# Kernel optimization log

Measured on AMD Instinct MI355X. Metric: run time of the kernel, lower is better.

Reference implementation:

```python
import jax, jax.numpy as jnp
import numpy as np

NU = 50000   # n_users
NI = 50000   # n_items
N = NU + NI  # total nodes in the square normalized adjacency
D = 64       # emb_dim
K = 4        # number of sub-graphs in hypergraph_list
E = 1000000  # interactions per sub-graph (symmetrized -> 2E nnz)


def setup_inputs() -> dict:
    key = jax.random.key(0)
    ks = jax.random.split(key, 9)
    stdv = 1.0 / np.sqrt(D)
    return {
        "x": jax.random.normal(ks[0], (N, D), jnp.float32),
        "hgc1_bias": jax.random.uniform(ks[1], (D,), jnp.float32, -stdv, stdv),
        "fc1_W": jax.random.normal(ks[2], (D, D), jnp.float32) * stdv,
        "fus_l1_W": jax.random.normal(ks[3], (D, D), jnp.float32) * stdv,
        "fus_l1_b": jnp.zeros((D,), jnp.float32),
        "fus_l2_W": jax.random.normal(ks[4], (1, D), jnp.float32) * stdv,
        "fus_l2_b": jnp.zeros((1,), jnp.float32),
        "rows": jax.random.randint(ks[5], (K, E), 0, NU),
        "cols": jax.random.randint(ks[6], (K, E), 0, NI),
    }


def reference(x, hgc1_bias, fc1_W, fus_l1_W, fus_l1_b, fus_l2_W, fus_l2_b, rows, cols):
    def spmm(src, dst, val, h):
        # (L @ h)[i] = sum over nnz (src=i): val * h[dst]
        return jax.ops.segment_sum(val[:, None] * h[dst], src, num_segments=N)

    def step(xc, rc):
        r, c = rc
        # symmetric bipartite adjacency A (items offset by NU)
        src = jnp.concatenate([r, c + NU])  # (2E,)
        dst = jnp.concatenate([c + NU, r])  # (2E,)
        # D^-1/2 A D^-1/2  (degree = row nnz count, as in (A>0).sum)
        deg = jax.ops.segment_sum(jnp.ones(src.shape, jnp.float32), src, num_segments=N) + 1e-7
        dinv = deg ** -0.5
        val = dinv[src] * dinv[dst]
        # HGNN2: relu -> hgc1 (bias add, edge=G^T x, x=G edge; G symmetric) -> softmax -> fc1
        h = jax.nn.relu(xc) + hgc1_bias
        edge = spmm(src, dst, val, h)
        node = spmm(src, dst, val, edge)
        node = jax.nn.softmax(node, axis=1)
        node = node @ fc1_W.T  # fc1 has no bias
        # Fusion gate (dropout off in eval)
        emb = jnp.stack([xc, node])  # (2, N, D)
        score = jax.nn.softmax(
            jnp.tanh(emb @ fus_l1_W.T + fus_l1_b) @ fus_l2_W.T + fus_l2_b, axis=0
        )  # (2, N, 1)
        x_new = jnp.sum(score * emb, axis=0)
        return x_new, (x_new, edge)

    _, (nodes, edges) = jax.lax.scan(step, x, (rows, cols))
    # embedding_list[sub_key] = [x, edge] per sub-graph -> stacked (K, N, D)
    return nodes, edges
```

## Files before the change

### kernel.cpp

```cpp
#include <hip/hip_runtime.h>
#include <hip/hip_bf16.h>

#define NU_ 50000
#define NI_ 50000
#define NN  (NU_ + NI_)
#define DD  64
#define KK  4
#define EE  1000000
#define SCAN_B ((NN + 255) / 256)

#define P_RANGES 8
#define RANGE_SZ ((NN + P_RANGES - 1) / P_RANGES)

__global__ __launch_bounds__(256) void k_hist(const int* __restrict__ rows,
                                              const int* __restrict__ cols,
                                              int* __restrict__ cnt4) {
    const int k = blockIdx.y;
    int e = blockIdx.x * 256 + threadIdx.x;
    if (e >= EE) return;
    int a = rows[(size_t)k * EE + e], b = cols[(size_t)k * EE + e];
    if ((unsigned)a >= (unsigned)NU_ || (unsigned)b >= (unsigned)NI_) return;
    int* cnt = cnt4 + (size_t)k * NN;
    atomicAdd(&cnt[a], 1);
    atomicAdd(&cnt[NU_ + b], 1);
}

__global__ __launch_bounds__(256) void k_bsum(const int* __restrict__ cnt4,
                                              int* __restrict__ bsum4) {
    __shared__ int s[256];
    const int k = blockIdx.y;
    int i = blockIdx.x * 256 + threadIdx.x;
    s[threadIdx.x] = (i < NN) ? cnt4[(size_t)k * NN + i] : 0;
    __syncthreads();
    #pragma unroll
    for (int off = 128; off > 0; off >>= 1) {
        if (threadIdx.x < off) s[threadIdx.x] += s[threadIdx.x + off];
        __syncthreads();
    }
    if (threadIdx.x == 0) bsum4[k * SCAN_B + blockIdx.x] = s[0];
}

__global__ __launch_bounds__(512) void k_sscan(const int* __restrict__ bsum4,
                                               int* __restrict__ bofs4) {
    __shared__ int s[512];
    const int k = blockIdx.x;
    int tid = threadIdx.x;
    s[tid] = (tid < SCAN_B) ? bsum4[k * SCAN_B + tid] : 0;
    __syncthreads();
    #pragma unroll
    for (int off = 1; off < 512; off <<= 1) {
        int v = (tid >= off) ? s[tid - off] : 0;
        __syncthreads();
        s[tid] += v;
        __syncthreads();
    }
    if (tid < SCAN_B) bofs4[k * SCAN_B + tid] = (tid > 0) ? s[tid - 1] : 0;
}

__global__ __launch_bounds__(256) void k_apply(const int* __restrict__ cnt4,
                                               const int* __restrict__ bofs4,
                                               int* __restrict__ row_ptr4,
                                               int* __restrict__ cursor4,
                                               float* __restrict__ dinv4) {
    __shared__ int s[256];
    const int k = blockIdx.y;
    int i = blockIdx.x * 256 + threadIdx.x;
    int v = (i < NN) ? cnt4[(size_t)k * NN + i] : 0;
    s[threadIdx.x] = v;
    __syncthreads();
    #pragma unroll
    for (int off = 1; off < 256; off <<= 1) {
        int t = (threadIdx.x >= off) ? s[threadIdx.x - off] : 0;
        __syncthreads();
        s[threadIdx.x] += t;
        __syncthreads();
    }
    if (i < NN) {
        int incl = s[threadIdx.x] + bofs4[k * SCAN_B + blockIdx.x];
        int excl = incl - v;
        row_ptr4[(size_t)k * (NN + 1) + i] = excl;
        cursor4[(size_t)k * NN + i] = excl;
        dinv4[(size_t)k * NN + i] = rsqrtf((float)v + 1e-7f);
        if (i == NN - 1) row_ptr4[(size_t)k * (NN + 1) + NN] = incl;
    }
}

__global__ __launch_bounds__(256) void k_scatter2(const int* __restrict__ rows,
                                                  const int* __restrict__ cols,
                                                  int* __restrict__ cursor4,
                                                  int* __restrict__ adj4) {
    const int g = blockIdx.x;
    const int k = blockIdx.z;
    const int lo = g * RANGE_SZ;
    int e = blockIdx.y * 256 + threadIdx.x;
    if (e >= EE) return;
    int a = rows[(size_t)k * EE + e], b = cols[(size_t)k * EE + e];
    if ((unsigned)a >= (unsigned)NU_ || (unsigned)b >= (unsigned)NI_) return;
    b += NU_;
    int* cursor = cursor4 + (size_t)k * NN;
    int* adj = adj4 + (size_t)k * 2 * EE;
    if ((unsigned)(a - lo) < (unsigned)RANGE_SZ) {
        int p = atomicAdd(&cursor[a], 1);
        adj[p] = b;
    }
    if ((unsigned)(b - lo) < (unsigned)RANGE_SZ) {
        int q = atomicAdd(&cursor[b], 1);
        adj[q] = a;
    }
}

__global__ __launch_bounds__(256) void k_prep(const float* __restrict__ x,
                                              const float* __restrict__ bias,
                                              const float* __restrict__ dinv,
                                              float* __restrict__ hbuf) {
    int i = blockIdx.x * 256 + threadIdx.x;
    int node = i >> 4;
    float dv = dinv[node];
    const float4 xv = ((const float4*)x)[i];
    const float4 bv = ((const float4*)bias)[i & 15];
    float4 o;
    o.x = dv * (fmaxf(xv.x, 0.f) + bv.x);
    o.y = dv * (fmaxf(xv.y, 0.f) + bv.y);
    o.z = dv * (fmaxf(xv.z, 0.f) + bv.z);
    o.w = dv * (fmaxf(xv.w, 0.f) + bv.w);
    ((float4*)hbuf)[i] = o;
}

__global__ __launch_bounds__(256) void k_pullA(const int* __restrict__ row_ptr,
                                               const int* __restrict__ adj,
                                               const float* __restrict__ dinv,
                                               const float* __restrict__ hbuf,
                                               float* __restrict__ out_e,
                                               float* __restrict__ h2buf) {
    const int wave = threadIdx.x >> 6;
    const int lane = threadIdx.x & 63;
    const int sub  = lane >> 4;
    const int l16  = lane & 15;
    const int lb   = sub << 4;
    const int row  = (blockIdx.x * 4 + wave) * 4 + sub;
    const int start = row_ptr[row];
    const int end   = row_ptr[row + 1];
    float4 aA = {0,0,0,0}, aB = {0,0,0,0};
    for (int base = start; base < end; base += 16) {
        int n = end - base; if (n > 16) n = 16;
        int idx = (l16 < n) ? adj[base + l16] : 0;
        int j = 0;
        for (; j + 3 < n; j += 4) {
            int n0 = __shfl(idx, lb | j);
            int n1 = __shfl(idx, lb | (j + 1));
            int n2 = __shfl(idx, lb | (j + 2));
            int n3 = __shfl(idx, lb | (j + 3));
            const float4 v0 = *(const float4*)&hbuf[(size_t)n0 * DD + l16 * 4];
            const float4 v1 = *(const float4*)&hbuf[(size_t)n1 * DD + l16 * 4];
            const float4 v2 = *(const float4*)&hbuf[(size_t)n2 * DD + l16 * 4];
            const float4 v3 = *(const float4*)&hbuf[(size_t)n3 * DD + l16 * 4];
            aA.x += v0.x; aA.y += v0.y; aA.z += v0.z; aA.w += v0.w;
            aB.x += v1.x; aB.y += v1.y; aB.z += v1.z; aB.w += v1.w;
            aA.x += v2.x; aA.y += v2.y; aA.z += v2.z; aA.w += v2.w;
            aB.x += v3.x; aB.y += v3.y; aB.z += v3.z; aB.w += v3.w;
        }
        for (; j < n; j++) {
            int nb = __shfl(idx, lb | j);
            const float4 v = *(const float4*)&hbuf[(size_t)nb * DD + l16 * 4];
            aA.x += v.x; aA.y += v.y; aA.z += v.z; aA.w += v.w;
        }
    }
    float4 acc = {aA.x + aB.x, aA.y + aB.y, aA.z + aB.z, aA.w + aB.w};
    const float dr = dinv[row];
    float4 e = {dr * acc.x, dr * acc.y, dr * acc.z, dr * acc.w};
    *(float4*)&out_e[(size_t)row * DD + l16 * 4] = e;
    float4 e2 = {dr * e.x, dr * e.y, dr * e.z, dr * e.w};
    *(float4*)&h2buf[(size_t)row * DD + l16 * 4] = e2;
}

__global__ __launch_bounds__(256) void k_pullB(const int* __restrict__ row_ptr,
                                               const int* __restrict__ adj,
                                               const float* __restrict__ dinv,
                                               const float* __restrict__ h2buf,
                                               float* __restrict__ out_n) {
    const int wave = threadIdx.x >> 6;
    const int lane = threadIdx.x & 63;
    const int sub  = lane >> 4;
    const int l16  = lane & 15;
    const int lb   = sub << 4;
    const int row  = (blockIdx.x * 4 + wave) * 4 + sub;
    const int start = row_ptr[row];
    const int end   = row_ptr[row + 1];
    float4 aA = {0,0,0,0}, aB = {0,0,0,0};
    for (int base = start; base < end; base += 16) {
        int n = end - base; if (n > 16) n = 16;
        int idx = (l16 < n) ? adj[base + l16] : 0;
        int j = 0;
        for (; j + 3 < n; j += 4) {
            int n0 = __shfl(idx, lb | j);
            int n1 = __shfl(idx, lb | (j + 1));
            int n2 = __shfl(idx, lb | (j + 2));
            int n3 = __shfl(idx, lb | (j + 3));
            const float4 v0 = *(const float4*)&h2buf[(size_t)n0 * DD + l16 * 4];
            const float4 v1 = *(const float4*)&h2buf[(size_t)n1 * DD + l16 * 4];
            const float4 v2 = *(const float4*)&h2buf[(size_t)n2 * DD + l16 * 4];
            const float4 v3 = *(const float4*)&h2buf[(size_t)n3 * DD + l16 * 4];
            aA.x += v0.x; aA.y += v0.y; aA.z += v0.z; aA.w += v0.w;
            aB.x += v1.x; aB.y += v1.y; aB.z += v1.z; aB.w += v1.w;
            aA.x += v2.x; aA.y += v2.y; aA.z += v2.z; aA.w += v2.w;
            aB.x += v3.x; aB.y += v3.y; aB.z += v3.z; aB.w += v3.w;
        }
        for (; j < n; j++) {
            int nb = __shfl(idx, lb | j);
            const float4 v = *(const float4*)&h2buf[(size_t)nb * DD + l16 * 4];
            aA.x += v.x; aA.y += v.y; aA.z += v.z; aA.w += v.w;
        }
    }
    float4 acc = {aA.x + aB.x, aA.y + aB.y, aA.z + aB.z, aA.w + aB.w};
    const float dr = dinv[row];
    float4 o = {dr * acc.x, dr * acc.y, dr * acc.z, dr * acc.w};
    *(float4*)&out_n[(size_t)row * DD + l16 * 4] = o;
}

#define BC(v, d) __uint_as_float(__builtin_amdgcn_readlane(__float_as_uint(v), (d)))

__global__ __launch_bounds__(256) void k_row(
    const float* __restrict__ node, const float* __restrict__ xsrc,
    const float* __restrict__ fc1W, const float* __restrict__ fusW,
    const float* __restrict__ l1b, const float* __restrict__ l2w,
    const float* __restrict__ l2b, const float* __restrict__ hgb,
    const float* __restrict__ dinv_next, float* __restrict__ out_nodes,
    float* __restrict__ hbuf_next) {
    const int wave = threadIdx.x >> 6;
    const int lane = threadIdx.x & 63;

    float wf[DD], wu[DD];
    #pragma unroll
    for (int d = 0; d < DD; d += 4) {
        *(float4*)&wf[d] = *(const float4*)&fc1W[(size_t)lane * DD + d];
        *(float4*)&wu[d] = *(const float4*)&fusW[(size_t)lane * DD + d];
    }
    const float b1v = l1b[lane];
    const float l2v = l2w[lane];
    const float b2v = l2b[0];
    const float hgv = hgb[lane];

    for (int row = blockIdx.x * 4 + wave; row < NN; row += gridDim.x * 4) {
        const size_t base = (size_t)row * DD + lane;
        float v = node[base];
        float m = v;
        #pragma unroll
        for (int s = 1; s < 64; s <<= 1) m = fmaxf(m, __shfl_xor(m, s));
        float ev = __expf(v - m);
        float sum = ev;
        #pragma unroll
        for (int s = 1; s < 64; s <<= 1) sum += __shfl_xor(sum, s);
        float sm = ev / sum;
        float n0 = 0, n1 = 0, n2 = 0, n3 = 0;
        #pragma unroll
        for (int d = 0; d < DD; d += 4) {
            n0 = fmaf(BC(sm, d),     wf[d],     n0);
            n1 = fmaf(BC(sm, d + 1), wf[d + 1], n1);
            n2 = fmaf(BC(sm, d + 2), wf[d + 2], n2);
            n3 = fmaf(BC(sm, d + 3), wf[d + 3], n3);
        }
        float nf = (n0 + n1) + (n2 + n3);
        float xc = xsrc[base];
        float a0 = 0, a1 = 0, a2 = 0, a3 = 0;
        #pragma unroll
        for (int d = 0; d < DD; d += 4) {
            a0 = fmaf(BC(xc, d),     wu[d],     a0);
            a1 = fmaf(BC(xc, d + 1), wu[d + 1], a1);
            a2 = fmaf(BC(xc, d + 2), wu[d + 2], a2);
            a3 = fmaf(BC(xc, d + 3), wu[d + 3], a3);
        }
        float tt = tanhf(((a0 + a1) + (a2 + a3)) + b1v);
        float p = tt * l2v;
        #pragma unroll
        for (int s = 1; s < 64; s <<= 1) p += __shfl_xor(p, s);
        float s_x = p + b2v;
        a0 = 0; a1 = 0; a2 = 0; a3 = 0;
        #pragma unroll
        for (int d = 0; d < DD; d += 4) {
            a0 = fmaf(BC(nf, d),     wu[d],     a0);
            a1 = fmaf(BC(nf, d + 1), wu[d + 1], a1);
            a2 = fmaf(BC(nf, d + 2), wu[d + 2], a2);
            a3 = fmaf(BC(nf, d + 3), wu[d + 3], a3);
        }
        tt = tanhf(((a0 + a1) + (a2 + a3)) + b1v);
        p = tt * l2v;
        #pragma unroll
        for (int s = 1; s < 64; s <<= 1) p += __shfl_xor(p, s);
        float s_n = p + b2v;
        float mm = fmaxf(s_x, s_n);
        float e0 = __expf(s_x - mm), e1 = __expf(s_n - mm);
        float inv = 1.0f / (e0 + e1);
        float xn = (e0 * xc + e1 * nf) * inv;
        out_nodes[base] = xn;
        if (hbuf_next) {
            float dv = dinv_next[row];
            hbuf_next[base] = dv * (fmaxf(xn, 0.f) + hgv);
        }
    }
}

extern "C" void kernel_launch(void* const* d_in, const int* in_sizes, int n_in,
                              void* d_out, int out_size, void* d_ws, size_t ws_size,
                              hipStream_t stream) {
    const float* x    = (const float*)d_in[0];
    const float* b1   = (const float*)d_in[1];
    const float* fc1W = (const float*)d_in[2];
    const float* fusW = (const float*)d_in[3];
    const float* l1b  = (const float*)d_in[4];
    const float* l2w  = (const float*)d_in[5];
    const float* l2b  = (const float*)d_in[6];
    const int* rows = (const int*)d_in[7];
    const int* cols = (const int*)d_in[8];
    float* out = (float*)d_out;

    const int ND = NN * DD;

    float* hbuf     = (float*)d_ws;
    float* h2buf    = hbuf + (size_t)NN * DD;
    float* dinv4    = h2buf + (size_t)NN * DD;
    int*   cnt4     = (int*)(dinv4 + (size_t)4 * NN);
    int*   row_ptr4 = cnt4 + (size_t)4 * NN;
    int*   cursor4  = row_ptr4 + (size_t)4 * (NN + 1);
    int*   bsum4    = cursor4 + (size_t)4 * NN;
    int*   bofs4    = bsum4 + 4 * SCAN_B;
    int*   adj4     = bofs4 + 4 * SCAN_B;

    hipMemsetAsync(cnt4, 0, (size_t)4 * NN * sizeof(int), stream);
    {
        dim3 g((EE + 255) / 256, KK);
        k_hist<<<g, 256, 0, stream>>>(rows, cols, cnt4);
    }
    {
        dim3 g(SCAN_B, KK);
        k_bsum<<<g, 256, 0, stream>>>(cnt4, bsum4);
    }
    k_sscan<<<KK, 512, 0, stream>>>(bsum4, bofs4);
    {
        dim3 g(SCAN_B, KK);
        k_apply<<<g, 256, 0, stream>>>(cnt4, bofs4, row_ptr4, cursor4, dinv4);
    }
    {
        dim3 g(P_RANGES, (EE + 255) / 256, KK);
        k_scatter2<<<g, 256, 0, stream>>>(rows, cols, cursor4, adj4);
    }

    k_prep<<<ND / 4 / 256, 256, 0, stream>>>(x, b1, dinv4, hbuf);

    for (int k = 0; k < KK; k++) {
        const int*   rp = row_ptr4 + (size_t)k * (NN + 1);
        const int*   aj = adj4 + (size_t)k * 2 * EE;
        const float* dv = dinv4 + (size_t)k * NN;
        const float* xk = (k == 0) ? x : out + (size_t)(k - 1) * ND;
        float* out_n = out + (size_t)k * ND;
        float* out_e = out + (size_t)(KK + k) * ND;

        k_pullA<<<NN / 16, 256, 0, stream>>>(rp, aj, dv, hbuf, out_e, h2buf);

        k_pullB<<<NN / 16, 256, 0, stream>>>(rp, aj, dv, h2buf, out_n);

        const float* dvn = (k < KK - 1) ? dinv4 + (size_t)(k + 1) * NN : nullptr;
        float* hbn = (k < KK - 1) ? hbuf : nullptr;
        k_row<<<1024, 256, 0, stream>>>(out_n, xk, fc1W, fusW, l1b, l2w, l2b,
                                        b1, dvn, out_n, hbn);
    }
}
```

Baseline: 1.793 ms.

## Range-partition histogram atomics, split scatter launches, widen gather accumulators

The degree histogram is now partitioned over node ranges like the scatter, so each block only issues atomics for nodes in its range, which improves atomic locality in cache. The scatter is split into two launches of two sub-graphs each. The SpMM gather loop gets a fully unrolled path for full 16-neighbour chunks and four independent accumulators to raise memory-level parallelism. In exchange, the histogram rereads the edge list once per range, and the extra accumulators raise register pressure.

```diff
diff --git a/kernel.cpp b/kernel.cpp
--- a/kernel.cpp
+++ b/kernel.cpp
@@ -12,17 +12,20 @@
 #define P_RANGES 8
 #define RANGE_SZ ((NN + P_RANGES - 1) / P_RANGES)
 
-__global__ __launch_bounds__(256) void k_hist(const int* __restrict__ rows,
-                                              const int* __restrict__ cols,
-                                              int* __restrict__ cnt4) {
-    const int k = blockIdx.y;
-    int e = blockIdx.x * 256 + threadIdx.x;
+__global__ __launch_bounds__(256) void k_hist2(const int* __restrict__ rows,
+                                               const int* __restrict__ cols,
+                                               int* __restrict__ cnt4) {
+    const int g = blockIdx.x;
+    const int k = blockIdx.z;
+    const int lo = g * RANGE_SZ;
+    int e = blockIdx.y * 256 + threadIdx.x;
     if (e >= EE) return;
     int a = rows[(size_t)k * EE + e], b = cols[(size_t)k * EE + e];
     if ((unsigned)a >= (unsigned)NU_ || (unsigned)b >= (unsigned)NI_) return;
+    b += NU_;
     int* cnt = cnt4 + (size_t)k * NN;
-    atomicAdd(&cnt[a], 1);
-    atomicAdd(&cnt[NU_ + b], 1);
+    if ((unsigned)(a - lo) < (unsigned)RANGE_SZ) atomicAdd(&cnt[a], 1);
+    if ((unsigned)(b - lo) < (unsigned)RANGE_SZ) atomicAdd(&cnt[b], 1);
 }
 
 __global__ __launch_bounds__(256) void k_bsum(const int* __restrict__ cnt4,
@@ -88,9 +91,10 @@
 __global__ __launch_bounds__(256) void k_scatter2(const int* __restrict__ rows,
                                                   const int* __restrict__ cols,
                                                   int* __restrict__ cursor4,
-                                                  int* __restrict__ adj4) {
+                                                  int* __restrict__ adj4,
+                                                  int kbase) {
     const int g = blockIdx.x;
-    const int k = blockIdx.z;
+    const int k = kbase + blockIdx.z;
     const int lo = g * RANGE_SZ;
     int e = blockIdx.y * 256 + threadIdx.x;
     if (e >= EE) return;
@@ -126,6 +130,55 @@
     ((float4*)hbuf)[i] = o;
 }
 
+#define GATHER_ROW(SRC, accOut)                                                \
+    float4 aA = {0,0,0,0}, aB = {0,0,0,0}, aC = {0,0,0,0}, aD = {0,0,0,0};     \
+    for (int base = start; base < end; base += 16) {                           \
+        int n = end - base; if (n > 16) n = 16;                                \
+        int idx = (l16 < n) ? adj[base + l16] : 0;                             \
+        if (n == 16) {                                                         \
+            _Pragma("unroll")                                                  \
+            for (int j = 0; j < 16; j += 4) {                                  \
+                int n0 = __shfl(idx, lb | j);                                  \
+                int n1 = __shfl(idx, lb | (j + 1));                            \
+                int n2 = __shfl(idx, lb | (j + 2));                            \
+                int n3 = __shfl(idx, lb | (j + 3));                            \
+                const float4 v0 = *(const float4*)&SRC[(size_t)n0 * DD + l16 * 4]; \
+                const float4 v1 = *(const float4*)&SRC[(size_t)n1 * DD + l16 * 4]; \
+                const float4 v2 = *(const float4*)&SRC[(size_t)n2 * DD + l16 * 4]; \
+                const float4 v3 = *(const float4*)&SRC[(size_t)n3 * DD + l16 * 4]; \
+                aA.x += v0.x; aA.y += v0.y; aA.z += v0.z; aA.w += v0.w;        \
+                aB.x += v1.x; aB.y += v1.y; aB.z += v1.z; aB.w += v1.w;        \
+                aC.x += v2.x; aC.y += v2.y; aC.z += v2.z; aC.w += v2.w;        \
+                aD.x += v3.x; aD.y += v3.y; aD.z += v3.z; aD.w += v3.w;        \
+            }                                                                  \
+        } else {                                                               \
+            int j = 0;                                                         \
+            for (; j + 3 < n; j += 4) {                                        \
+                int n0 = __shfl(idx, lb | j);                                  \
+                int n1 = __shfl(idx, lb | (j + 1));                            \
+                int n2 = __shfl(idx, lb | (j + 2));                            \
+                int n3 = __shfl(idx, lb | (j + 3));                            \
+                const float4 v0 = *(const float4*)&SRC[(size_t)n0 * DD + l16 * 4]; \
+                const float4 v1 = *(const float4*)&SRC[(size_t)n1 * DD + l16 * 4]; \
+                const float4 v2 = *(const float4*)&SRC[(size_t)n2 * DD + l16 * 4]; \
+                const float4 v3 = *(const float4*)&SRC[(size_t)n3 * DD + l16 * 4]; \
+                aA.x += v0.x; aA.y += v0.y; aA.z += v0.z; aA.w += v0.w;        \
+                aB.x += v1.x; aB.y += v1.y; aB.z += v1.z; aB.w += v1.w;        \
+                aC.x += v2.x; aC.y += v2.y; aC.z += v2.z; aC.w += v2.w;        \
+                aD.x += v3.x; aD.y += v3.y; aD.z += v3.z; aD.w += v3.w;        \
+            }                                                                  \
+            for (; j < n; j++) {                                               \
+                int nb = __shfl(idx, lb | j);                                  \
+                const float4 v = *(const float4*)&SRC[(size_t)nb * DD + l16 * 4]; \
+                aA.x += v.x; aA.y += v.y; aA.z += v.z; aA.w += v.w;            \
+            }                                                                  \
+        }                                                                      \
+    }                                                                          \
+    float4 accOut = {(aA.x + aB.x) + (aC.x + aD.x),                            \
+                     (aA.y + aB.y) + (aC.y + aD.y),                            \
+                     (aA.z + aB.z) + (aC.z + aD.z),                            \
+                     (aA.w + aB.w) + (aC.w + aD.w)};
+
 __global__ __launch_bounds__(256) void k_pullA(const int* __restrict__ row_ptr,
                                                const int* __restrict__ adj,
                                                const float* __restrict__ dinv,
@@ -140,32 +193,7 @@
     const int row  = (blockIdx.x * 4 + wave) * 4 + sub;
     const int start = row_ptr[row];
     const int end   = row_ptr[row + 1];
-    float4 aA = {0,0,0,0}, aB = {0,0,0,0};
-    for (int base = start; base < end; base += 16) {
-        int n = end - base; if (n > 16) n = 16;
-        int idx = (l16 < n) ? adj[base + l16] : 0;
-        int j = 0;
-        for (; j + 3 < n; j += 4) {
-            int n0 = __shfl(idx, lb | j);
-            int n1 = __shfl(idx, lb | (j + 1));
-            int n2 = __shfl(idx, lb | (j + 2));
-            int n3 = __shfl(idx, lb | (j + 3));
-            const float4 v0 = *(const float4*)&hbuf[(size_t)n0 * DD + l16 * 4];
-            const float4 v1 = *(const float4*)&hbuf[(size_t)n1 * DD + l16 * 4];
-            const float4 v2 = *(const float4*)&hbuf[(size_t)n2 * DD + l16 * 4];
-            const float4 v3 = *(const float4*)&hbuf[(size_t)n3 * DD + l16 * 4];
-            aA.x += v0.x; aA.y += v0.y; aA.z += v0.z; aA.w += v0.w;
-            aB.x += v1.x; aB.y += v1.y; aB.z += v1.z; aB.w += v1.w;
-            aA.x += v2.x; aA.y += v2.y; aA.z += v2.z; aA.w += v2.w;
-            aB.x += v3.x; aB.y += v3.y; aB.z += v3.z; aB.w += v3.w;
-        }
-        for (; j < n; j++) {
-            int nb = __shfl(idx, lb | j);
-            const float4 v = *(const float4*)&hbuf[(size_t)nb * DD + l16 * 4];
-            aA.x += v.x; aA.y += v.y; aA.z += v.z; aA.w += v.w;
-        }
-    }
-    float4 acc = {aA.x + aB.x, aA.y + aB.y, aA.z + aB.z, aA.w + aB.w};
+    GATHER_ROW(hbuf, acc)
     const float dr = dinv[row];
     float4 e = {dr * acc.x, dr * acc.y, dr * acc.z, dr * acc.w};
     *(float4*)&out_e[(size_t)row * DD + l16 * 4] = e;
@@ -186,32 +214,7 @@
     const int row  = (blockIdx.x * 4 + wave) * 4 + sub;
     const int start = row_ptr[row];
     const int end   = row_ptr[row + 1];
-    float4 aA = {0,0,0,0}, aB = {0,0,0,0};
-    for (int base = start; base < end; base += 16) {
-        int n = end - base; if (n > 16) n = 16;
-        int idx = (l16 < n) ? adj[base + l16] : 0;
-        int j = 0;
-        for (; j + 3 < n; j += 4) {
-            int n0 = __shfl(idx, lb | j);
-            int n1 = __shfl(idx, lb | (j + 1));
-            int n2 = __shfl(idx, lb | (j + 2));
-            int n3 = __shfl(idx, lb | (j + 3));
-            const float4 v0 = *(const float4*)&h2buf[(size_t)n0 * DD + l16 * 4];
-            const float4 v1 = *(const float4*)&h2buf[(size_t)n1 * DD + l16 * 4];
-            const float4 v2 = *(const float4*)&h2buf[(size_t)n2 * DD + l16 * 4];
-            const float4 v3 = *(const float4*)&h2buf[(size_t)n3 * DD + l16 * 4];
-            aA.x += v0.x; aA.y += v0.y; aA.z += v0.z; aA.w += v0.w;
-            aB.x += v1.x; aB.y += v1.y; aB.z += v1.z; aB.w += v1.w;
-            aA.x += v2.x; aA.y += v2.y; aA.z += v2.z; aA.w += v2.w;
-            aB.x += v3.x; aB.y += v3.y; aB.z += v3.z; aB.w += v3.w;
-        }
-        for (; j < n; j++) {
-            int nb = __shfl(idx, lb | j);
-            const float4 v = *(const float4*)&h2buf[(size_t)nb * DD + l16 * 4];
-            aA.x += v.x; aA.y += v.y; aA.z += v.z; aA.w += v.w;
-        }
-    }
-    float4 acc = {aA.x + aB.x, aA.y + aB.y, aA.z + aB.z, aA.w + aB.w};
+    GATHER_ROW(h2buf, acc)
     const float dr = dinv[row];
     float4 o = {dr * acc.x, dr * acc.y, dr * acc.z, dr * acc.w};
     *(float4*)&out_n[(size_t)row * DD + l16 * 4] = o;
@@ -327,8 +330,8 @@
 
     hipMemsetAsync(cnt4, 0, (size_t)4 * NN * sizeof(int), stream);
     {
-        dim3 g((EE + 255) / 256, KK);
-        k_hist<<<g, 256, 0, stream>>>(rows, cols, cnt4);
+        dim3 g(P_RANGES, (EE + 255) / 256, KK);
+        k_hist2<<<g, 256, 0, stream>>>(rows, cols, cnt4);
     }
     {
         dim3 g(SCAN_B, KK);
@@ -340,8 +343,9 @@
         k_apply<<<g, 256, 0, stream>>>(cnt4, bofs4, row_ptr4, cursor4, dinv4);
     }
     {
-        dim3 g(P_RANGES, (EE + 255) / 256, KK);
-        k_scatter2<<<g, 256, 0, stream>>>(rows, cols, cursor4, adj4);
+        dim3 g(P_RANGES, (EE + 255) / 256, 2);
+        k_scatter2<<<g, 256, 0, stream>>>(rows, cols, cursor4, adj4, 0);
+        k_scatter2<<<g, 256, 0, stream>>>(rows, cols, cursor4, adj4, 2);
     }
 
     k_prep<<<ND / 4 / 256, 256, 0, stream>>>(x, b1, dinv4, hbuf);
```

Result: no change. 1.813 ms (+1.1%).
